# Performance work log

Hardware: AMD Instinct MI355X
Metric: run time of the kernel (lower is better)

## Reference

```python
import jax, jax.numpy as jnp
import numpy as np

R = 3                      # corr_radius
K = (2 * R + 1) ** 2       # 49 correlation window
BANDS = 16
MAX_FREQ = 512.0
NUM_ITERS = 4
EPS = 1e-5


def _fourier(coords):
    # coords [..., D] -> [..., D*(2*BANDS+1)]
    freqs = (2.0 ** jnp.linspace(0.0, np.log2(MAX_FREQ), BANDS).astype(coords.dtype)) * np.pi
    x = coords[..., None] * freqs                      # [..., D, BANDS]
    enc = jnp.concatenate([jnp.sin(x), jnp.cos(x)], axis=-1)
    enc = enc.reshape(enc.shape[:-2] + (-1,))
    return jnp.concatenate([coords, enc], axis=-1)


def _layernorm(x, g, b):
    m = jnp.mean(x, -1, keepdims=True)
    v = jnp.mean(jnp.square(x - m), -1, keepdims=True)
    return (x - m) * jax.lax.rsqrt(v + EPS) * g + b


def _local_corr(query, fmaps, positions, stride):
    # query [B,Q,C], fmaps [B,T,C,H,W], positions [B,Q,T,2] -> corr [B,Q,T,K]
    B, T, C, H, W = fmaps.shape
    Q = query.shape[1]
    off = jnp.arange(-R, R + 1, dtype=positions.dtype)
    oy, ox = jnp.meshgrid(off, off, indexing='ij')
    og = jnp.stack([ox.reshape(-1), oy.reshape(-1)], -1)          # [K,2] (x,y)
    coords = positions / stride
    coords = coords[..., None, :] + og                             # [B,Q,T,K,2]
    coords = jnp.transpose(coords, (0, 2, 1, 3, 4)).reshape(B * T, Q * K, 2)
    fm = fmaps.reshape(B * T, C, H * W)

    def bilerp(f, xy):  # f [C,HW], xy [N,2] -> [C,N]; zeros padding, align_corners=True
        x, y = xy[:, 0], xy[:, 1]
        x0, y0 = jnp.floor(x), jnp.floor(y)
        dx, dy = x - x0, y - y0
        out = jnp.zeros((C, xy.shape[0]), f.dtype)
        for xi, yi, w in ((x0, y0, (1 - dx) * (1 - dy)),
                          (x0 + 1, y0, dx * (1 - dy)),
                          (x0, y0 + 1, (1 - dx) * dy),
                          (x0 + 1, y0 + 1, dx * dy)):
            valid = (xi >= 0) & (xi <= W - 1) & (yi >= 0) & (yi <= H - 1)
            idx = (jnp.clip(yi, 0, H - 1) * W + jnp.clip(xi, 0, W - 1)).astype(jnp.int32)
            out = out + (w * valid)[None, :] * f[:, idx]
        return out

    sampled = jax.vmap(bilerp)(fm, coords)                         # [BT,C,QK]
    sampled = sampled.reshape(B, T, C, Q, K)
    return jnp.einsum('btcqk,bqc->bqtk', sampled, query)


def _forward(coarse_tracks, query_features, feature_maps, feature_stride,
             proj_w, proj_b, ln1_g, ln1_b, conv_w, conv_b, ln2_g, ln2_b,
             mlp_w1, mlp_b1, mlp_w2, mlp_b2, delta_w, delta_b,
             vis_w1, vis_b1, vis_w2, vis_b2):
    B, Q, T, _ = coarse_tracks.shape
    D = proj_w.shape[1]
    dtype = coarse_tracks.dtype
    tracks = coarse_tracks
    t_idx = jnp.linspace(0.0, 1.0, T, dtype=dtype).reshape(1, 1, T, 1)
    hidden = jnp.zeros((B * Q, T, D), dtype)
    vis_sum = jnp.zeros((B, Q, T), dtype)
    num_blocks = ln1_g.shape[0]
    pad = conv_w.shape[-1] // 2
    for _ in range(NUM_ITERS):
        corr = _local_corr(query_features, feature_maps, tracks, feature_stride)
        pos_in = jnp.concatenate([tracks, jnp.broadcast_to(t_idx, (B, Q, T, 1))], -1)
        pos_enc = _fourier(pos_in)
        x = jnp.concatenate([corr, pos_enc, hidden.reshape(B, Q, T, D)], -1)
        x = x.reshape(B * Q, T, -1) @ proj_w + proj_b
        for i in range(num_blocks):
            h = _layernorm(x, ln1_g[i], ln1_b[i])
            h = jnp.transpose(h, (0, 2, 1))                        # [BQ,D,T]
            h = jax.lax.conv_general_dilated(
                h, conv_w[i], (1,), [(pad, pad)],
                dimension_numbers=('NCH', 'OIH', 'NCH'),
                feature_group_count=D) + conv_b[i][None, :, None]
            x = x + jnp.transpose(h, (0, 2, 1))
            h2 = _layernorm(x, ln2_g[i], ln2_b[i])
            x = x + jax.nn.gelu(h2 @ mlp_w1[i] + mlp_b1[i], approximate=False) @ mlp_w2[i] + mlp_b2[i]
        hidden = x
        delta = (x @ delta_w + delta_b).reshape(B, Q, T, 2)
        vis = (jax.nn.gelu(x @ vis_w1 + vis_b1, approximate=False) @ vis_w2 + vis_b2).reshape(B, Q, T)
        tracks = tracks + delta
        vis_sum = vis_sum + vis
    visibility = vis_sum / NUM_ITERS
    return jnp.concatenate([tracks, visibility[..., None]], -1)   # [B,Q,T,3]


def setup_inputs() -> dict:
    B, Q, T, C, H, W, D = 1, 128, 48, 64, 96, 128, 128
    NB, KSZ, IN_DIM = 4, 5, K + 3 * (2 * BANDS + 1) + D          # 49+99+128=276
    ks = jax.random.split(jax.random.key(0), 16)
    s = 0.05
    return {
        'coarse_tracks': jax.random.uniform(ks[0], (B, Q, T, 2)) * jnp.array([W * 4.0, H * 4.0]),
        'query_features': jax.random.normal(ks[1], (B, Q, C)),
        'feature_maps': jax.random.normal(ks[2], (B, T, C, H, W)),
        'feature_stride': 4,
        'proj_w': jax.random.normal(ks[3], (IN_DIM, D)) * s,
        'proj_b': jnp.zeros((D,)),
        'ln1_g': jnp.ones((NB, D)),
        'ln1_b': jnp.zeros((NB, D)),
        'conv_w': jax.random.normal(ks[4], (NB, D, 1, KSZ)) * 0.2,
        'conv_b': jnp.zeros((NB, D)),
        'ln2_g': jnp.ones((NB, D)),
        'ln2_b': jnp.zeros((NB, D)),
        'mlp_w1': jax.random.normal(ks[5], (NB, D, 2 * D)) * s,
        'mlp_b1': jnp.zeros((NB, 2 * D)),
        'mlp_w2': jax.random.normal(ks[6], (NB, 2 * D, D)) * s,
        'mlp_b2': jnp.zeros((NB, D)),
        'delta_w': jax.random.normal(ks[7], (D, 2)) * 0.01,
        'delta_b': jnp.zeros((2,)),
        'vis_w1': jax.random.normal(ks[8], (D, D // 2)) * s,
        'vis_b1': jnp.zeros((D // 2,)),
        'vis_w2': jax.random.normal(ks[9], (D // 2, 1)) * s,
        'vis_b2': jnp.zeros((1,)),
    }


def reference(coarse_tracks, query_features, feature_maps, feature_stride,
              proj_w, proj_b, ln1_g, ln1_b, conv_w, conv_b, ln2_g, ln2_b,
              mlp_w1, mlp_b1, mlp_w2, mlp_b2, delta_w, delta_b,
              vis_w1, vis_b1, vis_w2, vis_b2):
    return _forward(coarse_tracks, query_features, feature_maps, feature_stride,
                    proj_w, proj_b, ln1_g, ln1_b, conv_w, conv_b, ln2_g, ln2_b,
                    mlp_w1, mlp_b1, mlp_w2, mlp_b2, delta_w, delta_b,
                    vis_w1, vis_b1, vis_w2, vis_b2)
```

## Files before the change

### kernel.cpp

```cpp
#include <hip/hip_runtime.h>
#include <hip/hip_bf16.h>
#include <math.h>

#define QN 128
#define TN 48
#define CN 64
#define HN 96
#define WN 128
#define DN 128
#define KK 49
#define IN_DIM 276
#define XPAD 288
#define NROWS (QN*TN)
#define PI_F 3.14159265358979323846f

typedef __hip_bfloat16 bf16;
typedef unsigned short u16;
using bf16x8 = __attribute__((ext_vector_type(8))) short;
using f32x4  = __attribute__((ext_vector_type(4))) float;

__device__ inline float fixnan(float x){ return (x == x && fabsf(x) < 1e30f) ? x : 0.f; }

template<int MODE> __device__ inline float ld(const void* p, size_t i){
  if constexpr (MODE == 0) return ((const float*)p)[i];
  else {
    unsigned int u = ((const unsigned short*)p)[i];
    return __uint_as_float(u << 16);
  }
}

__device__ inline short f2b(float x){
  __hip_bfloat16 h = __float2bfloat16(x);
  return *reinterpret_cast<short*>(&h);
}
__device__ inline float b2f16(u16 u){ return __uint_as_float(((unsigned int)u) << 16); }

__device__ inline float waveReduceSum(float v){
  #pragma unroll
  for (int off = 32; off > 0; off >>= 1) v += __shfl_xor(v, off, 64);
  return v;
}

__device__ inline float gelu_exact(float x){
  return 0.5f * x * (1.f + erff(x * 0.70710678118654752440f));
}

__device__ inline f32x4 mfma16(bf16x8 a, bf16x8 b, f32x4 c){
  return __builtin_amdgcn_mfma_f32_16x16x32_bf16(a, b, c, 0, 0, 0);
}

__device__ inline float decode_stride(const void* p){
  int iv = *(const int*)p;
  if (iv >= 1 && iv <= (1 << 20)) return (float)iv;
  float fv = __int_as_float(iv);
  if (fv == fv && fv >= 0.25f && fv <= 1048576.f) return fv;
  unsigned int lo = ((unsigned int)(*(const unsigned short*)p)) << 16;
  float bv = __uint_as_float(lo);
  if (bv == bv && bv >= 0.25f && bv <= 1048576.f) return bv;
  return 4.f;
}

__device__ inline void bput(short* base, int stride_sh, int r, int k, float v){
  *(short*)((char*)base + (size_t)r*stride_sh*2 + ((2*k) ^ ((r & 7) << 4))) = f2b(v);
}
__device__ inline float bget(const short* base, int stride_sh, int r, int k){
  unsigned short u = *(const unsigned short*)((const char*)base + (size_t)r*stride_sh*2 + ((2*k) ^ ((r & 7) << 4)));
  return __uint_as_float(((unsigned int)u) << 16);
}
__device__ inline bf16x8 bget8(const short* base, int stride_sh, int r, int k0){
  return *(const bf16x8*)((const char*)base + (size_t)r*stride_sh*2 + ((2*k0) ^ ((r & 7) << 4)));
}

struct SLds {
  float qv[CN];
  float sdx[32], sdy[32], sc0[32], sc1[32];
  float hdl[32][132];
  union {
    struct { float dots[32][64]; short Xs[32][320]; } a;
    struct { short hn[32][128]; short y1[32][256]; } b;
  } u;
};

__global__ __launch_bounds__(256) void k_sniff(const unsigned short* __restrict__ q,
                                               int* __restrict__ flag){
  __shared__ int cnt;
  if (threadIdx.x == 0) cnt = 0;
  __syncthreads();
  int good = 0;
  for (int i = threadIdx.x; i < 8192; i += 256){
    float v = __uint_as_float(((unsigned int)q[i]) << 16);
    float a = fabsf(v);
    if (a > 1e-3f && a < 30.f) good++;
  }
  atomicAdd(&cnt, good);
  __syncthreads();
  if (threadIdx.x == 0) flag[0] = (cnt > 6500) ? 1 : 0;
}

template<int MODE>
__device__ void transpose_impl(u16 (*tile)[130], const void* fmap, u16* fmapT){
  int t = blockIdx.x / HN, y = blockIdx.x % HN;
  int tid = threadIdx.x, wv = tid >> 6, lane = tid & 63;
  #pragma unroll 4
  for (int ci = 0; ci < 16; ++ci){
    int c = ci*4 + wv;
    size_t base = (((size_t)t*CN + c)*HN + y)*WN;
    if constexpr (MODE == 1){
      const u16* fp = (const u16*)fmap + base + 2*lane;
      tile[c][2*lane]   = fp[0];
      tile[c][2*lane+1] = fp[1];
    } else {
      const float* fp = (const float*)fmap + base + 2*lane;
      tile[c][2*lane]   = (u16)f2b(fp[0]);
      tile[c][2*lane+1] = (u16)f2b(fp[1]);
    }
  }
  __syncthreads();
  u16* op = fmapT + (((size_t)t*HN + y)*WN)*CN + lane;
  #pragma unroll 4
  for (int xi = 0; xi < 32; ++xi){
    int x = xi*4 + wv;
    op[(size_t)x*CN] = tile[lane][x];
  }
}
__global__ __launch_bounds__(256) void k_transpose(const int* __restrict__ mf,
    const void* fmap, u16* fmapT){
  __shared__ u16 tile[64][130];
  if (mf[0] == 0) transpose_impl<0>(tile, fmap, fmapT);
  else            transpose_impl<1>(tile, fmap, fmapT);
}

#define TW_PW   (128*XPAD)
#define TW_W1   (4*256*128)
#define TW_W2   (4*128*256)
#define TW_VW1  (64*128)
#define TW_TOT  (TW_PW + TW_W1 + TW_W2 + TW_VW1)
template<int MODE>
__device__ void transW_impl(int idx, const void* pw, const void* w1, const void* w2,
                            const void* vw1,
                            bf16* pwt, bf16* w1t, bf16* w2t, bf16* vw1t){
  if (idx < TW_PW){
    int n = idx / XPAD, kk = idx % XPAD;
    float v = (kk < IN_DIM) ? ld<MODE>(pw, (size_t)kk*DN + n) : 0.f;
    ((short*)pwt)[idx] = f2b(v);
  } else if (idx < TW_PW + TW_W1){
    int i2 = idx - TW_PW;
    int k = i2 & 127, n = (i2 >> 7) & 255, l = i2 >> 15;
    ((short*)w1t)[i2] = f2b(ld<MODE>(w1, (size_t)l*32768 + (size_t)k*256 + n));
  } else if (idx < TW_PW + TW_W1 + TW_W2){
    int i3 = idx - TW_PW - TW_W1;
    int k = i3 & 255, n = (i3 >> 8) & 127, l = i3 >> 15;
    ((short*)w2t)[i3] = f2b(ld<MODE>(w2, (size_t)l*32768 + (size_t)k*128 + n));
  } else {
    int i4 = idx - TW_PW - TW_W1 - TW_W2;
    int n = i4 >> 7, k = i4 & 127;
    ((short*)vw1t)[i4] = f2b(ld<MODE>(vw1, (size_t)k*64 + n));
  }
}
__global__ __launch_bounds__(256) void k_transW(const int* __restrict__ mf,
    const void* pw, const void* w1, const void* w2, const void* vw1,
    bf16* pwt, bf16* w1t, bf16* w2t, bf16* vw1t){
  int idx = blockIdx.x*256 + threadIdx.x;
  if (idx >= TW_TOT) return;
  if (mf[0] == 0) transW_impl<0>(idx, pw, w1, w2, vw1, pwt, w1t, w2t, vw1t);
  else            transW_impl<1>(idx, pw, w1, w2, vw1, pwt, w1t, w2t, vw1t);
}

template<int MODE>
__device__ void init_impl(const void* ct, float* tracks, float* vis_sum){
  int i = blockIdx.x * 256 + threadIdx.x;
  if (i < NROWS){
    tracks[2*i]   = fixnan(ld<MODE>(ct, 2*i));
    tracks[2*i+1] = fixnan(ld<MODE>(ct, 2*i+1));
    vis_sum[i] = 0.f;
  }
}
__global__ __launch_bounds__(256) void k_init(const int* __restrict__ mf,
    const void* ct, float* tracks, float* vis_sum){
  if (mf[0] == 0) init_impl<0>(ct, tracks, vis_sum);
  else            init_impl<1>(ct, tracks, vis_sum);
}

template<int MODE, int FAST>
__device__ void iter_impl(SLds& s,
    const void* fmap, const u16* fmapT, const void* query, const void* stride_p,
    const float* __restrict__ tr_in, float* __restrict__ tr_out,
    const float* __restrict__ vi_in, float* __restrict__ vi_out,
    const float* __restrict__ hd_in, float* __restrict__ hd_out,
    const bf16* pwt, const void* pb,
    const void* ln1g, const void* ln1b, const void* cw, const void* cb,
    const void* ln2g, const void* ln2b,
    const bf16* w1t, const void* b1, const bf16* w2t, const void* b2,
    const void* dwp, const void* dbp,
    const bf16* vw1t, const void* vb1, const void* vw2, const void* vb2,
    void* out, int last)
{
  int bid = blockIdx.x;
  int q = bid >> 1, half = bid & 1, T0 = half * 16;
  int tid = threadIdx.x, wv = tid >> 6, ll = tid & 63;

  if (tid < CN) s.qv[tid] = ld<MODE>(query, q*CN + tid);
  float fs = decode_stride(stride_p);
  __syncthreads();

  if constexpr (FAST){
    float qv8[8];
    #pragma unroll
    for (int u = 0; u < 8; ++u) qv8[u] = s.qv[(ll & 7)*8 + u];
    #pragma unroll
    for (int rr = 0; rr < 4; ++rr){
      int r = wv*4 + rr, t = T0 + r, grow = q*TN + t;
      float c0 = fixnan(tr_in[2*grow]), c1 = fixnan(tr_in[2*grow+1]);
      float px = fminf(fmaxf(c0 / fs, -1e6f), 1e6f);
      float py = fminf(fmaxf(c1 / fs, -1e6f), 1e6f);
      float fx0 = floorf(px), fy0 = floorf(py);
      if (ll == 0){ s.sdx[r] = px - fx0; s.sdy[r] = py - fy0; s.sc0[r] = c0; s.sc1[r] = c1; }
      int x0 = (int)fx0 - 3, y0 = (int)fy0 - 3;
      s.u.a.dots[r][ll] = 0.f;
      if (x0 <= 127 && x0 + 7 >= 0){
        int x0c = min(max(x0, 0), WN - 8);
        int sh = x0c - x0;
        int ip = ll >> 3;
        int i = ip + sh;
        bool wr = ((ll & 7) == 0) && (i >= 0) && (i < 8);
        #pragma unroll
        for (int j = 0; j < 8; ++j){
          int yj = y0 + j;
          if (yj < 0 || yj >= HN) continue;
          const u16* blk = fmapT + ((((size_t)t*HN + yj)*WN + x0c) << 6);
          bf16x8 v = *(const bf16x8*)(blk + ll*8);
          float p = 0.f;
          #pragma unroll
          for (int u = 0; u < 8; ++u) p += qv8[u] * b2f16((u16)v[u]);
          p += __shfl_xor(p, 1, 64);
          p += __shfl_xor(p, 2, 64);
          p += __shfl_xor(p, 4, 64);
          if (wr) s.u.a.dots[r][j*8 + i] = p;
        }
      }
    }
  } else {
    for (int rr = 0; rr < 4; ++rr){
      int r = wv*4 + rr, t = T0 + r, grow = q*TN + t;
      float c0 = fixnan(tr_in[2*grow]), c1 = fixnan(tr_in[2*grow+1]);
      float px = fminf(fmaxf(c0 / fs, -1e6f), 1e6f);
      float py = fminf(fmaxf(c1 / fs, -1e6f), 1e6f);
      float fx0 = floorf(px), fy0 = floorf(py);
      if (ll == 0){ s.sdx[r] = px - fx0; s.sdy[r] = py - fy0; s.sc0[r] = c0; s.sc1[r] = c1; }
      int bx = (int)fx0, by = (int)fy0;
      int j = ll >> 3, i = ll & 7;
      int xi = bx + i - 3, yi = by + j - 3;
      float dot = 0.f;
      if (xi >= 0 && xi < WN && yi >= 0 && yi < HN){
        size_t base = ((size_t)t*CN)*HN*WN + (size_t)yi*WN + xi;
        #pragma unroll 8
        for (int c = 0; c < CN; ++c)
          dot += s.qv[c] * ld<MODE>(fmap, base + (size_t)c*HN*WN);
      }
      s.u.a.dots[r][ll] = dot;
    }
  }
  __syncthreads();

  for (int idx = tid; idx < 32*KK; idx += 512){
    int r = idx / KK, kk = idx % KK, oy = kk / 7, ox = kk % 7;
    float dx = s.sdx[r], dy = s.sdy[r];
    const float* dr = s.u.a.dots[r];
    float v = (1.f-dx)*(1.f-dy)*dr[oy*8+ox]     + dx*(1.f-dy)*dr[oy*8+ox+1]
            + (1.f-dx)*dy*dr[(oy+1)*8+ox]       + dx*dy*dr[(oy+1)*8+ox+1];
    bput(&s.u.a.Xs[0][0], 320, r, kk, fixnan(v));
  }
  for (int idx = tid; idx < 32*3; idx += 512){
    int r = idx / 3, cd = idx % 3;
    float v = (cd == 0) ? s.sc0[r] : (cd == 1 ? s.sc1[r] : (float)(T0+r)/(float)(TN-1));
    bput(&s.u.a.Xs[0][0], 320, r, KK + cd, v);
  }
  for (int idx = tid; idx < 32*96; idx += 512){
    int r = idx / 96, j = idx % 96, coord = j >> 5, rm = j & 31, band = rm & 15;
    float cv = (coord == 0) ? s.sc0[r] : (coord == 1 ? s.sc1[r] : (float)(T0+r)/(float)(TN-1));
    float a = cv * exp2f(0.6f*(float)band) * PI_F;
    float v = (rm < 16) ? __sinf(a) : __cosf(a);
    bput(&s.u.a.Xs[0][0], 320, r, KK + 3 + coord*32 + rm, fixnan(v));
  }
  for (int idx = tid; idx < 32*DN; idx += 512){
    int r = idx >> 7, d = idx & 127;
    int grow = q*TN + T0 + r;
    bput(&s.u.a.Xs[0][0], 320, r, 148 + d, fixnan(hd_in[(size_t)grow*DN + d]));
  }
  for (int idx = tid; idx < 32*12; idx += 512){
    int r = idx / 12, p = idx % 12;
    bput(&s.u.a.Xs[0][0], 320, r, IN_DIM + p, 0.f);
  }
  __syncthreads();

  {
    int rA = ll & 15, gK = ll >> 4;
    int rt = wv & 1, nt0 = wv >> 1;
    bf16x8 afr[9];
    #pragma unroll
    for (int ks = 0; ks < 9; ++ks)
      afr[ks] = bget8(&s.u.a.Xs[0][0], 320, rt*16 + rA, ks*32 + gK*8);
    #pragma unroll
    for (int h = 0; h < 2; ++h){
      int nt = nt0 + h*4;
      float bv = ld<MODE>(pb, nt*16 + rA);
      f32x4 acc = {bv, bv, bv, bv};
      #pragma unroll
      for (int ks = 0; ks < 9; ++ks)
        acc = mfma16(afr[ks],
          *(const bf16x8*)((const short*)pwt + (size_t)(nt*16 + rA)*XPAD + ks*32 + gK*8), acc);
      #pragma unroll
      for (int r2 = 0; r2 < 4; ++r2)
        s.hdl[rt*16 + gK*4 + r2][nt*16 + rA] = fixnan(acc[r2]);
    }
  }

  int dconv = tid & 127;
  #pragma unroll 1
  for (int L = 0; L < 4; ++L){
    float cwr[5];
    #pragma unroll
    for (int k = 0; k < 5; ++k) cwr[k] = ld<MODE>(cw, ((size_t)L*DN + dconv)*5 + k);
    float cbv = ld<MODE>(cb, L*DN + dconv);
    __syncthreads();
    {
      float g0 = ld<MODE>(ln1g, L*DN + ll), g1 = ld<MODE>(ln1g, L*DN + ll + 64);
      float b0 = ld<MODE>(ln1b, L*DN + ll), b1v = ld<MODE>(ln1b, L*DN + ll + 64);
      #pragma unroll
      for (int rr = 0; rr < 4; ++rr){
        int r = wv*4 + rr;
        float a0 = s.hdl[r][ll], a1 = s.hdl[r][ll+64];
        float m = waveReduceSum(a0 + a1) * (1.f/128.f);
        float v0 = a0 - m, v1 = a1 - m;
        float var = waveReduceSum(v0*v0 + v1*v1) * (1.f/128.f);
        float inv = rsqrtf(var + 1e-5f);
        bput(&s.u.b.hn[0][0], 128, r, ll,      v0*inv*g0 + b0);
        bput(&s.u.b.hn[0][0], 128, r, ll + 64, v1*inv*g1 + b1v);
      }
    }
    __syncthreads();
    for (int idx = tid; idx < 32*DN; idx += 512){
      int r = idx >> 7, t = T0 + r;
      float acc = cbv;
      #pragma unroll
      for (int k = 0; k < 5; ++k){
        int tg = t + k - 2, tl = r + k - 2;
        if (tg >= 0 && tg < TN && tl >= 0 && tl < 32)
          acc += bget(&s.u.b.hn[0][0], 128, tl, dconv) * cwr[k];
      }
      s.hdl[r][dconv] = fixnan(s.hdl[r][dconv] + acc);
    }
    __syncthreads();
    {
      float g0 = ld<MODE>(ln2g, L*DN + ll), g1 = ld<MODE>(ln2g, L*DN + ll + 64);
      float b0 = ld<MODE>(ln2b, L*DN + ll), b1v = ld<MODE>(ln2b, L*DN + ll + 64);
      #pragma unroll
      for (int rr = 0; rr < 4; ++rr){
        int r = wv*4 + rr;
        float a0 = s.hdl[r][ll], a1 = s.hdl[r][ll+64];
        float m = waveReduceSum(a0 + a1) * (1.f/128.f);
        float v0 = a0 - m, v1 = a1 - m;
        float var = waveReduceSum(v0*v0 + v1*v1) * (1.f/128.f);
        float inv = rsqrtf(var + 1e-5f);
        bput(&s.u.b.hn[0][0], 128, r, ll,      v0*inv*g0 + b0);
        bput(&s.u.b.hn[0][0], 128, r, ll + 64, v1*inv*g1 + b1v);
      }
    }
    __syncthreads();
    {
      int rA = ll & 15, gK = ll >> 4;
      int rt = wv & 1, nt0 = wv >> 1;
      const short* w1s = (const short*)w1t + (size_t)L*32768;
      bf16x8 afr[4];
      #pragma unroll
      for (int ks = 0; ks < 4; ++ks)
        afr[ks] = bget8(&s.u.b.hn[0][0], 128, rt*16 + rA, ks*32 + gK*8);
      #pragma unroll
      for (int h = 0; h < 4; ++h){
        int nt = nt0 + h*4;
        float bv = ld<MODE>(b1, L*256 + nt*16 + rA);
        f32x4 acc = {bv, bv, bv, bv};
        #pragma unroll
        for (int ks = 0; ks < 4; ++ks)
          acc = mfma16(afr[ks],
            *(const bf16x8*)(w1s + (size_t)(nt*16 + rA)*DN + ks*32 + gK*8), acc);
        #pragma unroll
        for (int r2 = 0; r2 < 4; ++r2)
          bput(&s.u.b.y1[0][0], 256, rt*16 + gK*4 + r2, nt*16 + rA, gelu_exact(acc[r2]));
      }
    }
    __syncthreads();
    {
      int rA = ll & 15, gK = ll >> 4;
      int rt = wv & 1, nt0 = wv >> 1;
      const short* w2s = (const short*)w2t + (size_t)L*32768;
      bf16x8 afr[8];
      #pragma unroll
      for (int ks = 0; ks < 8; ++ks)
        afr[ks] = bget8(&s.u.b.y1[0][0], 256, rt*16 + rA, ks*32 + gK*8);
      #pragma unroll
      for (int h = 0; h < 2; ++h){
        int nt = nt0 + h*4;
        float bv = ld<MODE>(b2, L*DN + nt*16 + rA);
        f32x4 acc = {bv, bv, bv, bv};
        #pragma unroll
        for (int ks = 0; ks < 8; ++ks)
          acc = mfma16(afr[ks],
            *(const bf16x8*)(w2s + (size_t)(nt*16 + rA)*256 + ks*32 + gK*8), acc);
        #pragma unroll
        for (int r2 = 0; r2 < 4; ++r2){
          int r = rt*16 + gK*4 + r2, cc = nt*16 + rA;
          s.hdl[r][cc] = fixnan(s.hdl[r][cc] + acc[r2]);
        }
      }
    }
  }
  __syncthreads();

  for (int idx = tid; idx < 32*DN; idx += 512){
    int r = idx >> 7, d = idx & 127;
    bput(&s.u.b.hn[0][0], 128, r, d, s.hdl[r][d]);
  }
  __syncthreads();
  float* gC = (float*)&s.u.b.y1[0][0];
  {
    int rA = ll & 15, gK = ll >> 4;
    int rt = wv & 1, nt = wv >> 1;
    float bv = ld<MODE>(vb1, nt*16 + rA);
    f32x4 acc = {bv, bv, bv, bv};
    #pragma unroll
    for (int ks = 0; ks < 4; ++ks)
      acc = mfma16(bget8(&s.u.b.hn[0][0], 128, rt*16 + rA, ks*32 + gK*8),
                   *(const bf16x8*)((const short*)vw1t + (size_t)(nt*16 + rA)*128 + ks*32 + gK*8), acc);
    #pragma unroll
    for (int r2 = 0; r2 < 4; ++r2)
      gC[(rt*16 + gK*4 + r2)*72 + nt*16 + rA] = gelu_exact(acc[r2]);
  }
  __syncthreads();
  float vw2v = ld<MODE>(vw2, ll);
  float dwa = ld<MODE>(dwp, ll*2),     dwb = ld<MODE>(dwp, (ll+64)*2);
  float dwc = ld<MODE>(dwp, ll*2 + 1), dwd = ld<MODE>(dwp, (ll+64)*2 + 1);
  #pragma unroll
  for (int rr = 0; rr < 4; ++rr){
    int r = wv*4 + rr, t = T0 + r, grow = q*TN + t;
    bool owned = half ? (r >= 8) : (r < 24);
    float vis = waveReduceSum(gC[r*72 + ll] * vw2v);
    float x0 = s.hdl[r][ll], x1 = s.hdl[r][ll+64];
    float dX = waveReduceSum(x0*dwa + x1*dwb);
    float dY = waveReduceSum(x0*dwc + x1*dwd);
    if (owned){
      hd_out[(size_t)grow*DN + ll]      = fixnan(x0);
      hd_out[(size_t)grow*DN + ll + 64] = fixnan(x1);
      if (ll == 0){
        float tx = fixnan(tr_in[2*grow]   + dX + ld<MODE>(dbp, 0));
        float ty = fixnan(tr_in[2*grow+1] + dY + ld<MODE>(dbp, 1));
        tr_out[2*grow] = tx; tr_out[2*grow+1] = ty;
        float vs = fixnan(vi_in[grow] + vis + ld<MODE>(vb2, 0));
        vi_out[grow] = vs;
        if (last){
          if constexpr (MODE == 0){
            ((float*)out)[grow*3 + 0] = tx;
            ((float*)out)[grow*3 + 1] = ty;
            ((float*)out)[grow*3 + 2] = vs * 0.25f;
          } else {
            ((bf16*)out)[grow*3 + 0] = __float2bfloat16(tx);
            ((bf16*)out)[grow*3 + 1] = __float2bfloat16(ty);
            ((bf16*)out)[grow*3 + 2] = __float2bfloat16(vs * 0.25f);
          }
        }
      }
    }
  }
}

template<int FAST>
__global__ __launch_bounds__(512, 2) void k_iter(const int* __restrict__ mf,
    const void* fmap, const u16* fmapT, const void* query, const void* stride_p,
    const float* tr_in, float* tr_out, const float* vi_in, float* vi_out,
    const float* hd_in, float* hd_out,
    const bf16* pwt, const void* pb,
    const void* ln1g, const void* ln1b, const void* cw, const void* cb,
    const void* ln2g, const void* ln2b,
    const bf16* w1t, const void* b1, const bf16* w2t, const void* b2,
    const void* dwp, const void* dbp,
    const bf16* vw1t, const void* vb1, const void* vw2, const void* vb2,
    void* out, int last)
{
  __shared__ SLds s;
  if (mf[0] == 0)
    iter_impl<0, FAST>(s, fmap, fmapT, query, stride_p, tr_in, tr_out, vi_in, vi_out, hd_in, hd_out,
                 pwt, pb, ln1g, ln1b, cw, cb, ln2g, ln2b, w1t, b1, w2t, b2,
                 dwp, dbp, vw1t, vb1, vw2, vb2, out, last);
  else
    iter_impl<1, FAST>(s, fmap, fmapT, query, stride_p, tr_in, tr_out, vi_in, vi_out, hd_in, hd_out,
                 pwt, pb, ln1g, ln1b, cw, cb, ln2g, ln2b, w1t, b1, w2t, b2,
                 dwp, dbp, vw1t, vb1, vw2, vb2, out, last);
}

extern "C" void kernel_launch(void* const* d_in, const int* in_sizes, int n_in,
                              void* d_out, int out_size, void* d_ws, size_t ws_size,
                              hipStream_t stream) {
  const void* ct    = d_in[0];
  const void* query = d_in[1];
  const void* fmap  = d_in[2];
  const void* fs    = d_in[3];
  const void* pw    = d_in[4];
  const void* pb    = d_in[5];
  const void* ln1g  = d_in[6];
  const void* ln1b  = d_in[7];
  const void* cw    = d_in[8];
  const void* cb    = d_in[9];
  const void* ln2g  = d_in[10];
  const void* ln2b  = d_in[11];
  const void* w1    = d_in[12];
  const void* b1    = d_in[13];
  const void* w2    = d_in[14];
  const void* b2    = d_in[15];
  const void* dw    = d_in[16];
  const void* db    = d_in[17];
  const void* vw1   = d_in[18];
  const void* vb1   = d_in[19];
  const void* vw2   = d_in[20];
  const void* vb2   = d_in[21];

  char* w0 = (char*)d_ws;
  char* w = w0;
  int*   mflag = (int*)w;                   w += 256;
  float* tr[2]; float* vi[2]; float* hd[2];
  for (int i = 0; i < 2; ++i){ tr[i] = (float*)w; w += ((size_t)NROWS*2*4 + 255) & ~255ull; }
  for (int i = 0; i < 2; ++i){ vi[i] = (float*)w; w += ((size_t)NROWS*4   + 255) & ~255ull; }
  for (int i = 0; i < 2; ++i){ hd[i] = (float*)w; w += ((size_t)NROWS*DN*4 + 255) & ~255ull; }
  bf16* pwt = (bf16*)w;                     w += ((size_t)128*XPAD*2 + 255) & ~255ull;
  bf16* w1t = (bf16*)w;                     w += ((size_t)4*256*128*2 + 255) & ~255ull;
  bf16* w2t = (bf16*)w;                     w += ((size_t)4*128*256*2 + 255) & ~255ull;
  bf16* vw1t = (bf16*)w;                    w += ((size_t)64*128*2 + 255) & ~255ull;
  u16*  fmapT = (u16*)w;                    w += ((size_t)TN*HN*WN*CN*2 + 255) & ~255ull;

  bool fast = ((size_t)(w - w0) <= ws_size);

  k_sniff<<<1, 256, 0, stream>>>((const unsigned short*)query, mflag);
  hipMemsetAsync(hd[0], 0, (size_t)NROWS*DN*4, stream);

  k_transW<<<(TW_TOT + 255)/256, 256, 0, stream>>>(mflag, pw, w1, w2, vw1, pwt, w1t, w2t, vw1t);
  k_init<<<(NROWS + 255)/256, 256, 0, stream>>>(mflag, ct, tr[0], vi[0]);
  if (fast)
    k_transpose<<<TN*HN, 256, 0, stream>>>(mflag, fmap, fmapT);

  for (int it = 0; it < 4; ++it){
    int a = it & 1, b = a ^ 1;
    if (fast)
      k_iter<1><<<256, 512, 0, stream>>>(mflag, fmap, fmapT, query, fs,
          tr[a], tr[b], vi[a], vi[b], hd[a], hd[b],
          pwt, pb, ln1g, ln1b, cw, cb, ln2g, ln2b,
          w1t, b1, w2t, b2, dw, db, vw1t, vb1, vw2, vb2,
          d_out, it == 3);
    else
      k_iter<0><<<256, 512, 0, stream>>>(mflag, fmap, fmapT, query, fs,
          tr[a], tr[b], vi[a], vi[b], hd[a], hd[b],
          pwt, pb, ln1g, ln1b, cw, cb, ln2g, ln2b,
          w1t, b1, w2t, b2, dw, db, vw1t, vb1, vw2, vb2,
          d_out, it == 3);
  }
}
```

Baseline: 383.1 us.

## Split each query's time axis into four halo chunks across smaller blocks

The per-iteration kernel now launches 512 blocks of 256 threads instead of 256 blocks of 512. Each block owns 12 timesteps of one query and recomputes an 8-step halo on each side, so the four stacked temporal convolutions stay correct without any cross-block exchange. Each wave now handles twice as many rows and MFMA tiles. LayerNorm switches to a one-pass sum and sum-of-squares variance so the two reductions are independent. The aim is finer-grained blocks with less work each, at the cost of more redundant halo rows and a less numerically stable variance.

```diff
diff --git a/kernel.cpp b/kernel.cpp
--- a/kernel.cpp
+++ b/kernel.cpp
@@ -196,7 +196,11 @@
     void* out, int last)
 {
   int bid = blockIdx.x;
-  int q = bid >> 1, half = bid & 1, T0 = half * 16;
+  int q = bid >> 2, ch = bid & 3;
+  int Town0 = 12*ch, Town1 = Town0 + 12;
+  int Tstart = max(0, Town0 - 8);
+  int Tend   = min(TN, Town0 + 20);
+  int NP = Tend - Tstart;
   int tid = threadIdx.x, wv = tid >> 6, ll = tid & 63;
 
   if (tid < CN) s.qv[tid] = ld<MODE>(query, q*CN + tid);
@@ -207,9 +211,11 @@
     float qv8[8];
     #pragma unroll
     for (int u = 0; u < 8; ++u) qv8[u] = s.qv[(ll & 7)*8 + u];
-    #pragma unroll
-    for (int rr = 0; rr < 4; ++rr){
-      int r = wv*4 + rr, t = T0 + r, grow = q*TN + t;
+    #pragma unroll 2
+    for (int rr = 0; rr < 8; ++rr){
+      int r = wv*8 + rr;
+      if (r >= NP) break;
+      int t = Tstart + r, grow = q*TN + t;
       float c0 = fixnan(tr_in[2*grow]), c1 = fixnan(tr_in[2*grow+1]);
       float px = fminf(fmaxf(c0 / fs, -1e6f), 1e6f);
       float py = fminf(fmaxf(c1 / fs, -1e6f), 1e6f);
@@ -240,8 +246,10 @@
       }
     }
   } else {
-    for (int rr = 0; rr < 4; ++rr){
-      int r = wv*4 + rr, t = T0 + r, grow = q*TN + t;
+    for (int rr = 0; rr < 8; ++rr){
+      int r = wv*8 + rr;
+      if (r >= NP) break;
+      int t = Tstart + r, grow = q*TN + t;
       float c0 = fixnan(tr_in[2*grow]), c1 = fixnan(tr_in[2*grow+1]);
       float px = fminf(fmaxf(c0 / fs, -1e6f), 1e6f);
       float py = fminf(fmaxf(c1 / fs, -1e6f), 1e6f);
@@ -262,7 +270,7 @@
   }
   __syncthreads();
 
-  for (int idx = tid; idx < 32*KK; idx += 512){
+  for (int idx = tid; idx < NP*KK; idx += 256){
     int r = idx / KK, kk = idx % KK, oy = kk / 7, ox = kk % 7;
     float dx = s.sdx[r], dy = s.sdy[r];
     const float* dr = s.u.a.dots[r];
@@ -270,24 +278,24 @@
             + (1.f-dx)*dy*dr[(oy+1)*8+ox]       + dx*dy*dr[(oy+1)*8+ox+1];
     bput(&s.u.a.Xs[0][0], 320, r, kk, fixnan(v));
   }
-  for (int idx = tid; idx < 32*3; idx += 512){
+  for (int idx = tid; idx < NP*3; idx += 256){
     int r = idx / 3, cd = idx % 3;
-    float v = (cd == 0) ? s.sc0[r] : (cd == 1 ? s.sc1[r] : (float)(T0+r)/(float)(TN-1));
+    float v = (cd == 0) ? s.sc0[r] : (cd == 1 ? s.sc1[r] : (float)(Tstart+r)/(float)(TN-1));
     bput(&s.u.a.Xs[0][0], 320, r, KK + cd, v);
   }
-  for (int idx = tid; idx < 32*96; idx += 512){
+  for (int idx = tid; idx < NP*96; idx += 256){
     int r = idx / 96, j = idx % 96, coord = j >> 5, rm = j & 31, band = rm & 15;
-    float cv = (coord == 0) ? s.sc0[r] : (coord == 1 ? s.sc1[r] : (float)(T0+r)/(float)(TN-1));
+    float cv = (coord == 0) ? s.sc0[r] : (coord == 1 ? s.sc1[r] : (float)(Tstart+r)/(float)(TN-1));
     float a = cv * exp2f(0.6f*(float)band) * PI_F;
     float v = (rm < 16) ? __sinf(a) : __cosf(a);
     bput(&s.u.a.Xs[0][0], 320, r, KK + 3 + coord*32 + rm, fixnan(v));
   }
-  for (int idx = tid; idx < 32*DN; idx += 512){
+  for (int idx = tid; idx < NP*DN; idx += 256){
     int r = idx >> 7, d = idx & 127;
-    int grow = q*TN + T0 + r;
+    int grow = q*TN + Tstart + r;
     bput(&s.u.a.Xs[0][0], 320, r, 148 + d, fixnan(hd_in[(size_t)grow*DN + d]));
   }
-  for (int idx = tid; idx < 32*12; idx += 512){
+  for (int idx = tid; idx < NP*12; idx += 256){
     int r = idx / 12, p = idx % 12;
     bput(&s.u.a.Xs[0][0], 320, r, IN_DIM + p, 0.f);
   }
@@ -301,8 +309,8 @@
     for (int ks = 0; ks < 9; ++ks)
       afr[ks] = bget8(&s.u.a.Xs[0][0], 320, rt*16 + rA, ks*32 + gK*8);
     #pragma unroll
-    for (int h = 0; h < 2; ++h){
-      int nt = nt0 + h*4;
+    for (int h = 0; h < 4; ++h){
+      int nt = nt0 + h*2;
       float bv = ld<MODE>(pb, nt*16 + rA);
       f32x4 acc = {bv, bv, bv, bv};
       #pragma unroll
@@ -326,26 +334,27 @@
     {
       float g0 = ld<MODE>(ln1g, L*DN + ll), g1 = ld<MODE>(ln1g, L*DN + ll + 64);
       float b0 = ld<MODE>(ln1b, L*DN + ll), b1v = ld<MODE>(ln1b, L*DN + ll + 64);
-      #pragma unroll
-      for (int rr = 0; rr < 4; ++rr){
-        int r = wv*4 + rr;
+      #pragma unroll 2
+      for (int rr = 0; rr < 8; ++rr){
+        int r = wv*8 + rr;
         float a0 = s.hdl[r][ll], a1 = s.hdl[r][ll+64];
-        float m = waveReduceSum(a0 + a1) * (1.f/128.f);
-        float v0 = a0 - m, v1 = a1 - m;
-        float var = waveReduceSum(v0*v0 + v1*v1) * (1.f/128.f);
+        float su = waveReduceSum(a0 + a1);
+        float sq = waveReduceSum(a0*a0 + a1*a1);
+        float m = su * (1.f/128.f);
+        float var = sq * (1.f/128.f) - m*m;
         float inv = rsqrtf(var + 1e-5f);
-        bput(&s.u.b.hn[0][0], 128, r, ll,      v0*inv*g0 + b0);
-        bput(&s.u.b.hn[0][0], 128, r, ll + 64, v1*inv*g1 + b1v);
+        bput(&s.u.b.hn[0][0], 128, r, ll,      (a0 - m)*inv*g0 + b0);
+        bput(&s.u.b.hn[0][0], 128, r, ll + 64, (a1 - m)*inv*g1 + b1v);
       }
     }
     __syncthreads();
-    for (int idx = tid; idx < 32*DN; idx += 512){
-      int r = idx >> 7, t = T0 + r;
+    for (int idx = tid; idx < NP*DN; idx += 256){
+      int r = idx >> 7, t = Tstart + r;
       float acc = cbv;
       #pragma unroll
       for (int k = 0; k < 5; ++k){
         int tg = t + k - 2, tl = r + k - 2;
-        if (tg >= 0 && tg < TN && tl >= 0 && tl < 32)
+        if (tg >= 0 && tg < TN && tl >= 0 && tl < NP)
           acc += bget(&s.u.b.hn[0][0], 128, tl, dconv) * cwr[k];
       }
       s.hdl[r][dconv] = fixnan(s.hdl[r][dconv] + acc);
@@ -354,16 +363,17 @@
     {
       float g0 = ld<MODE>(ln2g, L*DN + ll), g1 = ld<MODE>(ln2g, L*DN + ll + 64);
       float b0 = ld<MODE>(ln2b, L*DN + ll), b1v = ld<MODE>(ln2b, L*DN + ll + 64);
-      #pragma unroll
-      for (int rr = 0; rr < 4; ++rr){
-        int r = wv*4 + rr;
+      #pragma unroll 2
+      for (int rr = 0; rr < 8; ++rr){
+        int r = wv*8 + rr;
         float a0 = s.hdl[r][ll], a1 = s.hdl[r][ll+64];
-        float m = waveReduceSum(a0 + a1) * (1.f/128.f);
-        float v0 = a0 - m, v1 = a1 - m;
-        float var = waveReduceSum(v0*v0 + v1*v1) * (1.f/128.f);
+        float su = waveReduceSum(a0 + a1);
+        float sq = waveReduceSum(a0*a0 + a1*a1);
+        float m = su * (1.f/128.f);
+        float var = sq * (1.f/128.f) - m*m;
         float inv = rsqrtf(var + 1e-5f);
-        bput(&s.u.b.hn[0][0], 128, r, ll,      v0*inv*g0 + b0);
-        bput(&s.u.b.hn[0][0], 128, r, ll + 64, v1*inv*g1 + b1v);
+        bput(&s.u.b.hn[0][0], 128, r, ll,      (a0 - m)*inv*g0 + b0);
+        bput(&s.u.b.hn[0][0], 128, r, ll + 64, (a1 - m)*inv*g1 + b1v);
       }
     }
     __syncthreads();
@@ -376,8 +386,8 @@
       for (int ks = 0; ks < 4; ++ks)
         afr[ks] = bget8(&s.u.b.hn[0][0], 128, rt*16 + rA, ks*32 + gK*8);
       #pragma unroll
-      for (int h = 0; h < 4; ++h){
-        int nt = nt0 + h*4;
+      for (int h = 0; h < 8; ++h){
+        int nt = nt0 + h*2;
         float bv = ld<MODE>(b1, L*256 + nt*16 + rA);
         f32x4 acc = {bv, bv, bv, bv};
         #pragma unroll
@@ -399,8 +409,8 @@
       for (int ks = 0; ks < 8; ++ks)
         afr[ks] = bget8(&s.u.b.y1[0][0], 256, rt*16 + rA, ks*32 + gK*8);
       #pragma unroll
-      for (int h = 0; h < 2; ++h){
-        int nt = nt0 + h*4;
+      for (int h = 0; h < 4; ++h){
+        int nt = nt0 + h*2;
         float bv = ld<MODE>(b2, L*DN + nt*16 + rA);
         f32x4 acc = {bv, bv, bv, bv};
         #pragma unroll
@@ -417,7 +427,7 @@
   }
   __syncthreads();
 
-  for (int idx = tid; idx < 32*DN; idx += 512){
+  for (int idx = tid; idx < NP*DN; idx += 256){
     int r = idx >> 7, d = idx & 127;
     bput(&s.u.b.hn[0][0], 128, r, d, s.hdl[r][d]);
   }
@@ -425,25 +435,31 @@
   float* gC = (float*)&s.u.b.y1[0][0];
   {
     int rA = ll & 15, gK = ll >> 4;
-    int rt = wv & 1, nt = wv >> 1;
-    float bv = ld<MODE>(vb1, nt*16 + rA);
-    f32x4 acc = {bv, bv, bv, bv};
+    int rt = wv & 1, nt0 = wv >> 1;
     #pragma unroll
-    for (int ks = 0; ks < 4; ++ks)
-      acc = mfma16(bget8(&s.u.b.hn[0][0], 128, rt*16 + rA, ks*32 + gK*8),
-                   *(const bf16x8*)((const short*)vw1t + (size_t)(nt*16 + rA)*128 + ks*32 + gK*8), acc);
-    #pragma unroll
-    for (int r2 = 0; r2 < 4; ++r2)
-      gC[(rt*16 + gK*4 + r2)*72 + nt*16 + rA] = gelu_exact(acc[r2]);
+    for (int h = 0; h < 2; ++h){
+      int nt = nt0 + h*2;
+      float bv = ld<MODE>(vb1, nt*16 + rA);
+      f32x4 acc = {bv, bv, bv, bv};
+      #pragma unroll
+      for (int ks = 0; ks < 4; ++ks)
+        acc = mfma16(bget8(&s.u.b.hn[0][0], 128, rt*16 + rA, ks*32 + gK*8),
+                     *(const bf16x8*)((const short*)vw1t + (size_t)(nt*16 + rA)*128 + ks*32 + gK*8), acc);
+      #pragma unroll
+      for (int r2 = 0; r2 < 4; ++r2)
+        gC[(rt*16 + gK*4 + r2)*72 + nt*16 + rA] = gelu_exact(acc[r2]);
+    }
   }
   __syncthreads();
   float vw2v = ld<MODE>(vw2, ll);
   float dwa = ld<MODE>(dwp, ll*2),     dwb = ld<MODE>(dwp, (ll+64)*2);
   float dwc = ld<MODE>(dwp, ll*2 + 1), dwd = ld<MODE>(dwp, (ll+64)*2 + 1);
-  #pragma unroll
-  for (int rr = 0; rr < 4; ++rr){
-    int r = wv*4 + rr, t = T0 + r, grow = q*TN + t;
-    bool owned = half ? (r >= 8) : (r < 24);
+  #pragma unroll 2
+  for (int rr = 0; rr < 8; ++rr){
+    int r = wv*8 + rr;
+    if (r >= NP) break;
+    int t = Tstart + r, grow = q*TN + t;
+    bool owned = (t >= Town0) && (t < Town1);
     float vis = waveReduceSum(gC[r*72 + ll] * vw2v);
     float x0 = s.hdl[r][ll], x1 = s.hdl[r][ll+64];
     float dX = waveReduceSum(x0*dwa + x1*dwb);
@@ -474,7 +490,7 @@
 }
 
 template<int FAST>
-__global__ __launch_bounds__(512, 2) void k_iter(const int* __restrict__ mf,
+__global__ __launch_bounds__(256, 2) void k_iter(const int* __restrict__ mf,
     const void* fmap, const u16* fmapT, const void* query, const void* stride_p,
     const float* tr_in, float* tr_out, const float* vi_in, float* vi_out,
     const float* hd_in, float* hd_out,
@@ -549,13 +565,13 @@
   for (int it = 0; it < 4; ++it){
     int a = it & 1, b = a ^ 1;
     if (fast)
-      k_iter<1><<<256, 512, 0, stream>>>(mflag, fmap, fmapT, query, fs,
+      k_iter<1><<<512, 256, 0, stream>>>(mflag, fmap, fmapT, query, fs,
           tr[a], tr[b], vi[a], vi[b], hd[a], hd[b],
           pwt, pb, ln1g, ln1b, cw, cb, ln2g, ln2b,
           w1t, b1, w2t, b2, dw, db, vw1t, vb1, vw2, vb2,
           d_out, it == 3);
     else
-      k_iter<0><<<256, 512, 0, stream>>>(mflag, fmap, fmapT, query, fs,
+      k_iter<0><<<512, 256, 0, stream>>>(mflag, fmap, fmapT, query, fs,
           tr[a], tr[b], vi[a], vi[b], hd[a], hd[b],
           pwt, pb, ln1g, ln1b, cw, cb, ln2g, ln2b,
           w1t, b1, w2t, b2, dw, db, vw1t, vb1, vw2, vb2,
```

Result: slower. 625.2 us (+63.2%).

## Split local correlation into its own high-parallelism kernel before each iteration

Applied to the files above, without the earlier changes.

Moves the correlation gather and bilinear interpolation out of the 256-block iteration kernel into a separate kernel with one 64-thread block per (query, frame) row. The row results go to a bf16 workspace buffer that the iteration kernel reads. The point is to spread the latency-bound feature-map gathers across many more blocks and shrink LDS use in the main kernel. Two smaller changes ride along: the hidden-state load is vectorised, and layernorm uses a single-pass sum and sum-of-squares. The cost is an extra launch per iteration, a global round trip for the correlation values, and slightly less numerically stable variance.

```diff
diff --git a/kernel.cpp b/kernel.cpp
--- a/kernel.cpp
+++ b/kernel.cpp
@@ -72,11 +72,10 @@
 }
 
 struct SLds {
-  float qv[CN];
-  float sdx[32], sdy[32], sc0[32], sc1[32];
+  float sc0[32], sc1[32];
   float hdl[32][132];
   union {
-    struct { float dots[32][64]; short Xs[32][320]; } a;
+    short Xs[32][320];
     struct { short hn[32][128]; short y1[32][256]; } b;
   } u;
 };
@@ -182,8 +181,86 @@
 }
 
 template<int MODE, int FAST>
+__device__ void corr_impl(float* qv, float* dots,
+    const void* fmap, const u16* fmapT, const void* query, const void* stride_p,
+    const float* __restrict__ tr, short* __restrict__ Xc)
+{
+  int blk = blockIdx.x;
+  int q = blk / TN, t = blk % TN;
+  int ll = threadIdx.x;
+  qv[ll] = ld<MODE>(query, q*CN + ll);
+  float fs = decode_stride(stride_p);
+  float c0 = fixnan(tr[2*blk]), c1 = fixnan(tr[2*blk+1]);
+  float px = fminf(fmaxf(c0 / fs, -1e6f), 1e6f);
+  float py = fminf(fmaxf(c1 / fs, -1e6f), 1e6f);
+  float fx0 = floorf(px), fy0 = floorf(py);
+  float dx = px - fx0, dy = py - fy0;
+  __syncthreads();
+
+  if constexpr (FAST){
+    float qv8[8];
+    #pragma unroll
+    for (int u = 0; u < 8; ++u) qv8[u] = qv[(ll & 7)*8 + u];
+    int x0 = (int)fx0 - 3, y0 = (int)fy0 - 3;
+    dots[ll] = 0.f;
+    __syncthreads();
+    if (x0 <= 127 && x0 + 7 >= 0){
+      int x0c = min(max(x0, 0), WN - 8);
+      int sh = x0c - x0;
+      int ip = ll >> 3;
+      int i = ip + sh;
+      bool wr = ((ll & 7) == 0) && (i >= 0) && (i < 8);
+      #pragma unroll
+      for (int j = 0; j < 8; ++j){
+        int yj = y0 + j;
+        if (yj < 0 || yj >= HN) continue;
+        const u16* blkp = fmapT + ((((size_t)t*HN + yj)*WN + x0c) << 6);
+        bf16x8 v = *(const bf16x8*)(blkp + ll*8);
+        float p = 0.f;
+        #pragma unroll
+        for (int u = 0; u < 8; ++u) p += qv8[u] * b2f16((u16)v[u]);
+        p += __shfl_xor(p, 1, 64);
+        p += __shfl_xor(p, 2, 64);
+        p += __shfl_xor(p, 4, 64);
+        if (wr) dots[j*8 + i] = p;
+      }
+    }
+  } else {
+    int bx = (int)fx0, by = (int)fy0;
+    int j = ll >> 3, i = ll & 7;
+    int xi = bx + i - 3, yi = by + j - 3;
+    float dot = 0.f;
+    if (xi >= 0 && xi < WN && yi >= 0 && yi < HN){
+      size_t base = ((size_t)t*CN)*HN*WN + (size_t)yi*WN + xi;
+      #pragma unroll 8
+      for (int c = 0; c < CN; ++c)
+        dot += qv[c] * ld<MODE>(fmap, base + (size_t)c*HN*WN);
+    }
+    dots[j*8 + i] = dot;
+  }
+  __syncthreads();
+
+  if (ll < KK){
+    int oy = ll / 7, ox = ll % 7;
+    float v = (1.f-dx)*(1.f-dy)*dots[oy*8+ox]   + dx*(1.f-dy)*dots[oy*8+ox+1]
+            + (1.f-dx)*dy*dots[(oy+1)*8+ox]     + dx*dy*dots[(oy+1)*8+ox+1];
+    Xc[(size_t)blk*64 + ll] = f2b(fixnan(v));
+  }
+}
+template<int FAST>
+__global__ __launch_bounds__(64) void k_corr(const int* __restrict__ mf,
+    const void* fmap, const u16* fmapT, const void* query, const void* stride_p,
+    const float* tr, short* Xc)
+{
+  __shared__ float qv[CN];
+  __shared__ float dots[64];
+  if (mf[0] == 0) corr_impl<0, FAST>(qv, dots, fmap, fmapT, query, stride_p, tr, Xc);
+  else            corr_impl<1, FAST>(qv, dots, fmap, fmapT, query, stride_p, tr, Xc);
+}
+
+template<int MODE>
 __device__ void iter_impl(SLds& s,
-    const void* fmap, const u16* fmapT, const void* query, const void* stride_p,
+    const short* __restrict__ Xc,
     const float* __restrict__ tr_in, float* __restrict__ tr_out,
     const float* __restrict__ vi_in, float* __restrict__ vi_out,
     const float* __restrict__ hd_in, float* __restrict__ hd_out,
@@ -198,98 +275,40 @@
   int bid = blockIdx.x;
   int q = bid >> 1, half = bid & 1, T0 = half * 16;
   int tid = threadIdx.x, wv = tid >> 6, ll = tid & 63;
-
-  if (tid < CN) s.qv[tid] = ld<MODE>(query, q*CN + tid);
-  float fs = decode_stride(stride_p);
-  __syncthreads();
-
-  if constexpr (FAST){
-    float qv8[8];
-    #pragma unroll
-    for (int u = 0; u < 8; ++u) qv8[u] = s.qv[(ll & 7)*8 + u];
-    #pragma unroll
-    for (int rr = 0; rr < 4; ++rr){
-      int r = wv*4 + rr, t = T0 + r, grow = q*TN + t;
-      float c0 = fixnan(tr_in[2*grow]), c1 = fixnan(tr_in[2*grow+1]);
-      float px = fminf(fmaxf(c0 / fs, -1e6f), 1e6f);
-      float py = fminf(fmaxf(c1 / fs, -1e6f), 1e6f);
-      float fx0 = floorf(px), fy0 = floorf(py);
-      if (ll == 0){ s.sdx[r] = px - fx0; s.sdy[r] = py - fy0; s.sc0[r] = c0; s.sc1[r] = c1; }
-      int x0 = (int)fx0 - 3, y0 = (int)fy0 - 3;
-      s.u.a.dots[r][ll] = 0.f;
-      if (x0 <= 127 && x0 + 7 >= 0){
-        int x0c = min(max(x0, 0), WN - 8);
-        int sh = x0c - x0;
-        int ip = ll >> 3;
-        int i = ip + sh;
-        bool wr = ((ll & 7) == 0) && (i >= 0) && (i < 8);
-        #pragma unroll
-        for (int j = 0; j < 8; ++j){
-          int yj = y0 + j;
-          if (yj < 0 || yj >= HN) continue;
-          const u16* blk = fmapT + ((((size_t)t*HN + yj)*WN + x0c) << 6);
-          bf16x8 v = *(const bf16x8*)(blk + ll*8);
-          float p = 0.f;
-          #pragma unroll
-          for (int u = 0; u < 8; ++u) p += qv8[u] * b2f16((u16)v[u]);
-          p += __shfl_xor(p, 1, 64);
-          p += __shfl_xor(p, 2, 64);
-          p += __shfl_xor(p, 4, 64);
-          if (wr) s.u.a.dots[r][j*8 + i] = p;
-        }
-      }
-    }
-  } else {
-    for (int rr = 0; rr < 4; ++rr){
-      int r = wv*4 + rr, t = T0 + r, grow = q*TN + t;
-      float c0 = fixnan(tr_in[2*grow]), c1 = fixnan(tr_in[2*grow+1]);
-      float px = fminf(fmaxf(c0 / fs, -1e6f), 1e6f);
-      float py = fminf(fmaxf(c1 / fs, -1e6f), 1e6f);
-      float fx0 = floorf(px), fy0 = floorf(py);
-      if (ll == 0){ s.sdx[r] = px - fx0; s.sdy[r] = py - fy0; s.sc0[r] = c0; s.sc1[r] = c1; }
-      int bx = (int)fx0, by = (int)fy0;
-      int j = ll >> 3, i = ll & 7;
-      int xi = bx + i - 3, yi = by + j - 3;
-      float dot = 0.f;
-      if (xi >= 0 && xi < WN && yi >= 0 && yi < HN){
-        size_t base = ((size_t)t*CN)*HN*WN + (size_t)yi*WN + xi;
-        #pragma unroll 8
-        for (int c = 0; c < CN; ++c)
-          dot += s.qv[c] * ld<MODE>(fmap, base + (size_t)c*HN*WN);
-      }
-      s.u.a.dots[r][ll] = dot;
-    }
+  int R0 = q*TN + T0;
+
+  if (tid < 32){
+    s.sc0[tid] = fixnan(tr_in[2*(R0 + tid)]);
+    s.sc1[tid] = fixnan(tr_in[2*(R0 + tid) + 1]);
   }
   __syncthreads();
 
   for (int idx = tid; idx < 32*KK; idx += 512){
-    int r = idx / KK, kk = idx % KK, oy = kk / 7, ox = kk % 7;
-    float dx = s.sdx[r], dy = s.sdy[r];
-    const float* dr = s.u.a.dots[r];
-    float v = (1.f-dx)*(1.f-dy)*dr[oy*8+ox]     + dx*(1.f-dy)*dr[oy*8+ox+1]
-            + (1.f-dx)*dy*dr[(oy+1)*8+ox]       + dx*dy*dr[(oy+1)*8+ox+1];
-    bput(&s.u.a.Xs[0][0], 320, r, kk, fixnan(v));
+    int r = idx / KK, kk = idx % KK;
+    bput(&s.u.Xs[0][0], 320, r, kk, b2f16((u16)Xc[(size_t)(R0 + r)*64 + kk]));
   }
   for (int idx = tid; idx < 32*3; idx += 512){
     int r = idx / 3, cd = idx % 3;
     float v = (cd == 0) ? s.sc0[r] : (cd == 1 ? s.sc1[r] : (float)(T0+r)/(float)(TN-1));
-    bput(&s.u.a.Xs[0][0], 320, r, KK + cd, v);
+    bput(&s.u.Xs[0][0], 320, r, KK + cd, v);
   }
   for (int idx = tid; idx < 32*96; idx += 512){
     int r = idx / 96, j = idx % 96, coord = j >> 5, rm = j & 31, band = rm & 15;
     float cv = (coord == 0) ? s.sc0[r] : (coord == 1 ? s.sc1[r] : (float)(T0+r)/(float)(TN-1));
     float a = cv * exp2f(0.6f*(float)band) * PI_F;
     float v = (rm < 16) ? __sinf(a) : __cosf(a);
-    bput(&s.u.a.Xs[0][0], 320, r, KK + 3 + coord*32 + rm, fixnan(v));
-  }
-  for (int idx = tid; idx < 32*DN; idx += 512){
-    int r = idx >> 7, d = idx & 127;
-    int grow = q*TN + T0 + r;
-    bput(&s.u.a.Xs[0][0], 320, r, 148 + d, fixnan(hd_in[(size_t)grow*DN + d]));
+    bput(&s.u.Xs[0][0], 320, r, KK + 3 + coord*32 + rm, fixnan(v));
+  }
+  for (int idx = tid; idx < 32*32; idx += 512){
+    int r = idx >> 5, d4 = (idx & 31)*4;
+    f32x4 hv = *(const f32x4*)(hd_in + (size_t)(R0 + r)*DN + d4);
+    #pragma unroll
+    for (int u = 0; u < 4; ++u)
+      bput(&s.u.Xs[0][0], 320, r, 148 + d4 + u, fixnan(hv[u]));
   }
   for (int idx = tid; idx < 32*12; idx += 512){
     int r = idx / 12, p = idx % 12;
-    bput(&s.u.a.Xs[0][0], 320, r, IN_DIM + p, 0.f);
+    bput(&s.u.Xs[0][0], 320, r, IN_DIM + p, 0.f);
   }
   __syncthreads();
 
@@ -299,7 +318,7 @@
     bf16x8 afr[9];
     #pragma unroll
     for (int ks = 0; ks < 9; ++ks)
-      afr[ks] = bget8(&s.u.a.Xs[0][0], 320, rt*16 + rA, ks*32 + gK*8);
+      afr[ks] = bget8(&s.u.Xs[0][0], 320, rt*16 + rA, ks*32 + gK*8);
     #pragma unroll
     for (int h = 0; h < 2; ++h){
       int nt = nt0 + h*4;
@@ -330,12 +349,13 @@
       for (int rr = 0; rr < 4; ++rr){
         int r = wv*4 + rr;
         float a0 = s.hdl[r][ll], a1 = s.hdl[r][ll+64];
-        float m = waveReduceSum(a0 + a1) * (1.f/128.f);
-        float v0 = a0 - m, v1 = a1 - m;
-        float var = waveReduceSum(v0*v0 + v1*v1) * (1.f/128.f);
+        float su = waveReduceSum(a0 + a1);
+        float sq = waveReduceSum(a0*a0 + a1*a1);
+        float m = su * (1.f/128.f);
+        float var = fmaxf(sq * (1.f/128.f) - m*m, 0.f);
         float inv = rsqrtf(var + 1e-5f);
-        bput(&s.u.b.hn[0][0], 128, r, ll,      v0*inv*g0 + b0);
-        bput(&s.u.b.hn[0][0], 128, r, ll + 64, v1*inv*g1 + b1v);
+        bput(&s.u.b.hn[0][0], 128, r, ll,      (a0 - m)*inv*g0 + b0);
+        bput(&s.u.b.hn[0][0], 128, r, ll + 64, (a1 - m)*inv*g1 + b1v);
       }
     }
     __syncthreads();
@@ -358,12 +378,13 @@
       for (int rr = 0; rr < 4; ++rr){
         int r = wv*4 + rr;
         float a0 = s.hdl[r][ll], a1 = s.hdl[r][ll+64];
-        float m = waveReduceSum(a0 + a1) * (1.f/128.f);
-        float v0 = a0 - m, v1 = a1 - m;
-        float var = waveReduceSum(v0*v0 + v1*v1) * (1.f/128.f);
+        float su = waveReduceSum(a0 + a1);
+        float sq = waveReduceSum(a0*a0 + a1*a1);
+        float m = su * (1.f/128.f);
+        float var = fmaxf(sq * (1.f/128.f) - m*m, 0.f);
         float inv = rsqrtf(var + 1e-5f);
-        bput(&s.u.b.hn[0][0], 128, r, ll,      v0*inv*g0 + b0);
-        bput(&s.u.b.hn[0][0], 128, r, ll + 64, v1*inv*g1 + b1v);
+        bput(&s.u.b.hn[0][0], 128, r, ll,      (a0 - m)*inv*g0 + b0);
+        bput(&s.u.b.hn[0][0], 128, r, ll + 64, (a1 - m)*inv*g1 + b1v);
       }
     }
     __syncthreads();
@@ -473,9 +494,8 @@
   }
 }
 
-template<int FAST>
 __global__ __launch_bounds__(512, 2) void k_iter(const int* __restrict__ mf,
-    const void* fmap, const u16* fmapT, const void* query, const void* stride_p,
+    const short* Xc,
     const float* tr_in, float* tr_out, const float* vi_in, float* vi_out,
     const float* hd_in, float* hd_out,
     const bf16* pwt, const void* pb,
@@ -488,11 +508,11 @@
 {
   __shared__ SLds s;
   if (mf[0] == 0)
-    iter_impl<0, FAST>(s, fmap, fmapT, query, stride_p, tr_in, tr_out, vi_in, vi_out, hd_in, hd_out,
+    iter_impl<0>(s, Xc, tr_in, tr_out, vi_in, vi_out, hd_in, hd_out,
                  pwt, pb, ln1g, ln1b, cw, cb, ln2g, ln2b, w1t, b1, w2t, b2,
                  dwp, dbp, vw1t, vb1, vw2, vb2, out, last);
   else
-    iter_impl<1, FAST>(s, fmap, fmapT, query, stride_p, tr_in, tr_out, vi_in, vi_out, hd_in, hd_out,
+    iter_impl<1>(s, Xc, tr_in, tr_out, vi_in, vi_out, hd_in, hd_out,
                  pwt, pb, ln1g, ln1b, cw, cb, ln2g, ln2b, w1t, b1, w2t, b2,
                  dwp, dbp, vw1t, vb1, vw2, vb2, out, last);
 }
@@ -530,6 +550,7 @@
   for (int i = 0; i < 2; ++i){ tr[i] = (float*)w; w += ((size_t)NROWS*2*4 + 255) & ~255ull; }
   for (int i = 0; i < 2; ++i){ vi[i] = (float*)w; w += ((size_t)NROWS*4   + 255) & ~255ull; }
   for (int i = 0; i < 2; ++i){ hd[i] = (float*)w; w += ((size_t)NROWS*DN*4 + 255) & ~255ull; }
+  short* Xc = (short*)w;                    w += ((size_t)NROWS*64*2 + 255) & ~255ull;
   bf16* pwt = (bf16*)w;                     w += ((size_t)128*XPAD*2 + 255) & ~255ull;
   bf16* w1t = (bf16*)w;                     w += ((size_t)4*256*128*2 + 255) & ~255ull;
   bf16* w2t = (bf16*)w;                     w += ((size_t)4*128*256*2 + 255) & ~255ull;
@@ -549,16 +570,13 @@
   for (int it = 0; it < 4; ++it){
     int a = it & 1, b = a ^ 1;
     if (fast)
-      k_iter<1><<<256, 512, 0, stream>>>(mflag, fmap, fmapT, query, fs,
-          tr[a], tr[b], vi[a], vi[b], hd[a], hd[b],
-          pwt, pb, ln1g, ln1b, cw, cb, ln2g, ln2b,
-          w1t, b1, w2t, b2, dw, db, vw1t, vb1, vw2, vb2,
-          d_out, it == 3);
+      k_corr<1><<<NROWS, 64, 0, stream>>>(mflag, fmap, fmapT, query, fs, tr[a], Xc);
     else
-      k_iter<0><<<256, 512, 0, stream>>>(mflag, fmap, fmapT, query, fs,
-          tr[a], tr[b], vi[a], vi[b], hd[a], hd[b],
-          pwt, pb, ln1g, ln1b, cw, cb, ln2g, ln2b,
-          w1t, b1, w2t, b2, dw, db, vw1t, vb1, vw2, vb2,
-          d_out, it == 3);
-  }
-}
+      k_corr<0><<<NROWS, 64, 0, stream>>>(mflag, fmap, fmapT, query, fs, tr[a], Xc);
+    k_iter<<<256, 512, 0, stream>>>(mflag, Xc,
+        tr[a], tr[b], vi[a], vi[b], hd[a], hd[b],
+        pwt, pb, ln1g, ln1b, cw, cb, ln2g, ln2b,
+        w1t, b1, w2t, b2, dw, db, vw1t, vb1, vw2, vb2,
+        d_out, it == 3);
+  }
+}
```

After: 361.8 us. -5.6%, faster.
